# Kernel optimization log

Measured on AMD Instinct MI355X. Metric: run time of the kernel, lower is better.

Reference implementation:

```python
import jax, jax.numpy as jnp
import numpy as np

E = 1024   # embed_dim
H = 16     # num_heads
D = E // H # head_dim
NP = 2     # n_physics
PH = 16    # physics adapter hidden


def setup_inputs() -> dict:
    key = jax.random.key(0)
    ks = jax.random.split(key, 16)
    B, T = 2, 2048
    s = 0.02
    return {
        "x": jax.random.normal(ks[0], (B, T, E), dtype=jnp.float32),
        "physics_state": jax.random.uniform(ks[1], (B, NP), dtype=jnp.float32),
        "attn_mask": jax.random.randint(ks[2], (B, T), 0, 2).astype(jnp.bool_),
        "Wq": jax.random.normal(ks[3], (E, E), dtype=jnp.float32) * s,
        "bq": jnp.zeros((E,), dtype=jnp.float32),
        "Wk": jax.random.normal(ks[4], (E, E), dtype=jnp.float32) * s,
        "bk": jnp.zeros((E,), dtype=jnp.float32),
        "Wv": jax.random.normal(ks[5], (E, E), dtype=jnp.float32) * s,
        "bv": jnp.zeros((E,), dtype=jnp.float32),
        "Wo": jax.random.normal(ks[6], (E, E), dtype=jnp.float32) * s,
        "bo": jnp.zeros((E,), dtype=jnp.float32),
        "Wp1": jax.random.normal(ks[7], (NP, PH), dtype=jnp.float32) * 0.5,
        "bp1": jnp.zeros((PH,), dtype=jnp.float32),
        "Wp2": jax.random.normal(ks[8], (PH, H), dtype=jnp.float32) * 0.25,
        "bp2": jnp.zeros((H,), dtype=jnp.float32),
    }


def reference(x, physics_state, attn_mask, Wq, bq, Wk, bk, Wv, bv, Wo, bo, Wp1, bp1, Wp2, bp2):
    B, T, _ = x.shape
    scale = 1.0 / np.sqrt(D)
    # projections -> (B, H, T, D)
    q = (x @ Wq + bq).reshape(B, T, H, D).transpose(0, 2, 1, 3)
    k = (x @ Wk + bk).reshape(B, T, H, D).transpose(0, 2, 1, 3)
    v = (x @ Wv + bv).reshape(B, T, H, D).transpose(0, 2, 1, 3)
    # per-head physics bias (B, H) -> (B, H, 1, 1)
    h = jax.nn.gelu(physics_state @ Wp1 + bp1, approximate=False)
    phys_bias = (h @ Wp2 + bp2)[:, :, None, None]
    scores = jnp.einsum("bhqd,bhkd->bhqk", q, k) * scale + phys_bias
    # key padding mask: True = keep
    scores = jnp.where(attn_mask[:, None, None, :], scores, -jnp.inf)
    attn = jax.nn.softmax(scores, axis=-1)
    out = jnp.einsum("bhqk,bhkd->bhqd", attn, v)
    out = out.transpose(0, 2, 1, 3).reshape(B, T, E)
    return out @ Wo + bo
```

## Files before the change

### kernel.cpp

```cpp
#include <hip/hip_runtime.h>
#include <hip/hip_bf16.h>
#include <stdint.h>

#define E_  1024
#define H_  16
#define D_  64
#define T_  2048
#define B_  2

typedef unsigned short u16;
typedef unsigned char u8;
typedef __attribute__((ext_vector_type(8))) __bf16 bf16x8;
typedef __attribute__((ext_vector_type(4))) float f32x4;
typedef __attribute__((ext_vector_type(8))) u16 u16x8;
typedef __attribute__((ext_vector_type(4))) u16 u16x4;

__device__ __forceinline__ float bf2f(u16 u) {
  union { uint32_t u32; float f; } x; x.u32 = ((uint32_t)u) << 16; return x.f;
}
__device__ __forceinline__ u16 f2bf(float v) {
  union { float f; uint32_t u; } x; x.f = v;
  uint32_t r = x.u + 0x7fffu + ((x.u >> 16) & 1u);
  return (u16)(r >> 16);
}
__device__ __forceinline__ void async16(const void* g, void* l) {
  __builtin_amdgcn_global_load_lds(
      (const __attribute__((address_space(1))) void*)g,
      (__attribute__((address_space(3))) void*)l, 16, 0, 0);
}
__device__ __forceinline__ int jperm(int k) {
  return (k & 35) | ((k & 12) << 1) | ((k & 16) >> 2);
}

__device__ __forceinline__ int detect_f32(const void* src) {
  u16 u = ((const u16*)src)[2 * (threadIdx.x & 63)];
  int e = (u >> 7) & 0xFF;
  int ex = (e != 0 && (e <= 0x40 || e >= 0xC0)) ? 1 : 0;
  return __popcll(__ballot(ex)) > 16;
}

__global__ __launch_bounds__(256) void convf_kernel(const void* __restrict__ src,
                                                    u16* __restrict__ dst, int n) {
  const int f32in = detect_f32(src);
  int i = (blockIdx.x * 256 + threadIdx.x) * 8;
  if (i >= n) return;
  if (f32in) {
    const float* s = (const float*)src;
    u16x8 o;
#pragma unroll
    for (int j = 0; j < 8; ++j) o[j] = f2bf(s[i + j]);
    *(u16x8*)(dst + i) = o;
  } else {
    *(u16x8*)(dst + i) = *(const u16x8*)((const u16*)src + i);
  }
}

__global__ __launch_bounds__(256) void bias4_kernel(
    const void* __restrict__ b0, const void* __restrict__ b1,
    const void* __restrict__ b2, const void* __restrict__ b3,
    u16* __restrict__ dst) {
  const void* src = (blockIdx.x == 0) ? b0 : (blockIdx.x == 1) ? b1
                    : (blockIdx.x == 2) ? b2 : b3;
  const int f32in = detect_f32(src);
  u16* d = dst + blockIdx.x * 2048;
  int t = threadIdx.x;
#pragma unroll
  for (int j = 0; j < 4; ++j) {
    int i = t + j * 256;
    d[i] = f32in ? f2bf(((const float*)src)[i]) : ((const u16*)src)[i];
  }
}

__global__ __launch_bounds__(256) void maskbias_kernel(const void* __restrict__ mp,
                                                       float* __restrict__ mbg) {
  unsigned w0 = ((const unsigned*)mp)[threadIdx.x & 63];
  int isInt = (__ballot(w0 > 1u) == 0ull);
  int i = blockIdx.x * 256 + threadIdx.x;
  int keep = isInt ? (((const int*)mp)[i] != 0) : (((const u8*)mp)[i] != 0);
  mbg[i] = keep ? -5.77078016f : -30000.f;
}

__global__ __launch_bounds__(256) void wtc4_kernel(
    const void* __restrict__ W0, const void* __restrict__ W1,
    const void* __restrict__ W2, const void* __restrict__ W3,
    u16* __restrict__ T0, u16* __restrict__ T1,
    u16* __restrict__ T2, u16* __restrict__ T3) {
  __shared__ __align__(16) u16 tile[64][65];
  const int z = blockIdx.z;
  const void* Wv = (z == 0) ? W0 : (z == 1) ? W1 : (z == 2) ? W2 : W3;
  u16* WT = (z == 0) ? T0 : (z == 1) ? T1 : (z == 2) ? T2 : T3;
  const int f32in = detect_f32(Wv);
  const int bx = blockIdx.x * 64, by = blockIdx.y * 64;
  const int t = threadIdx.x;
#pragma unroll
  for (int p = 0; p < 2; ++p) {
    int row = p * 32 + (t >> 3);
    int ch = t & 7;
    if (f32in) {
      const float* s = (const float*)Wv + (size_t)(by + row) * E_ + bx + ch * 8;
#pragma unroll
      for (int j = 0; j < 8; ++j) tile[row][ch * 8 + j] = f2bf(s[j]);
    } else {
      u16x8 v = *(const u16x8*)((const u16*)Wv + (size_t)(by + row) * E_ + bx + ch * 8);
#pragma unroll
      for (int j = 0; j < 8; ++j) tile[row][ch * 8 + j] = v[j];
    }
  }
  __syncthreads();
#pragma unroll
  for (int p = 0; p < 2; ++p) {
    int orow = p * 32 + (t >> 3);
    int ch = t & 7;
    u16x8 v;
#pragma unroll
    for (int j = 0; j < 8; ++j) v[j] = tile[ch * 8 + j][orow];
    *(u16x8*)(WT + (size_t)(bx + orow) * E_ + by + ch * 8) = v;
  }
}

__global__ __launch_bounds__(256, 3) void gemm_qkv_kernel(
    const u16* __restrict__ A, const u16* __restrict__ BTm,
    const u16* __restrict__ biases, u16* __restrict__ Qb,
    u16* __restrict__ Kb, u16* __restrict__ Vtb) {
  __shared__ __align__(16) u16 As[128 * 64];
  __shared__ __align__(16) u16 Bs[128 * 64];
  const int tid = threadIdx.x, lane = tid & 63, wid = tid >> 6;
  const int wm = wid >> 1, wn = wid & 1;
  const int l15 = lane & 15, lg = lane >> 4;
  const int r0 = blockIdx.x * 128, c0 = blockIdx.y * 128;
  f32x4 acc[4][4] = {};

  for (int k0 = 0; k0 < E_; k0 += 64) {
    __syncthreads();
#pragma unroll
    for (int i = 0; i < 4; ++i) {
      int row = i * 32 + (tid >> 3);
      int g = (tid & 7) ^ (row & 7);
      async16(A + (size_t)(r0 + row) * E_ + k0 + g * 8,
              (char*)As + i * 4096 + tid * 16);
      async16(BTm + (size_t)(c0 + row) * E_ + k0 + g * 8,
              (char*)Bs + i * 4096 + tid * 16);
    }
    __syncthreads();
#pragma unroll
    for (int kk = 0; kk < 2; ++kk) {
      bf16x8 af[4], bfr[4];
#pragma unroll
      for (int mt = 0; mt < 4; ++mt) {
        int rowa = wm * 64 + mt * 16 + l15;
        int sa = (kk * 4 + lg) ^ (rowa & 7);
        af[mt] = *(const bf16x8*)((const char*)As + rowa * 128 + sa * 16);
        int rowb = wn * 64 + mt * 16 + l15;
        int sb = (kk * 4 + lg) ^ (rowb & 7);
        bfr[mt] = *(const bf16x8*)((const char*)Bs + rowb * 128 + sb * 16);
      }
#pragma unroll
      for (int mt = 0; mt < 4; ++mt)
#pragma unroll
        for (int nt = 0; nt < 4; ++nt)
          acc[mt][nt] = __builtin_amdgcn_mfma_f32_16x16x32_bf16(
              af[mt], bfr[nt], acc[mt][nt], 0, 0, 0);
    }
  }

  const int sel = c0 >> 10;
  u16* outp = (sel == 0) ? Qb : Kb;
#pragma unroll
  for (int mt = 0; mt < 4; ++mt) {
#pragma unroll
    for (int nt = 0; nt < 4; ++nt) {
      int colG = c0 + wn * 64 + nt * 16 + l15;
      int colL = colG & 1023;
      float bv = bf2f(biases[sel * 2048 + colL]);
      int rbase = r0 + wm * 64 + mt * 16 + lg * 4;
      int hh = colL >> 6, dd = colL & 63;
      if (sel == 2) {
        int bb = rbase >> 11, t0 = rbase & (T_ - 1);
        int tp = (t0 & ~63) | jperm(t0 & 63);
        u16x4 pk;
#pragma unroll
        for (int r = 0; r < 4; ++r) pk[r] = f2bf(acc[mt][nt][r] + bv);
        *(u16x4*)(Vtb + (size_t)((bb * H_ + hh) * D_ + dd) * T_ + tp) = pk;
      } else {
#pragma unroll
        for (int r = 0; r < 4; ++r) {
          int row = rbase + r;
          int bb = row >> 11, t = row & (T_ - 1);
          outp[(size_t)((bb * H_ + hh) * T_ + t) * D_ + dd] =
              f2bf(acc[mt][nt][r] + bv);
        }
      }
    }
  }
}

__global__ __launch_bounds__(256, 3) void gemm_out_kernel(
    const u16* __restrict__ A, const u16* __restrict__ BTm,
    const u16* __restrict__ bias, float* __restrict__ out) {
  __shared__ __align__(16) u16 As[128 * 64];
  __shared__ __align__(16) u16 Bs[128 * 64];
  const int tid = threadIdx.x, lane = tid & 63, wid = tid >> 6;
  const int wm = wid >> 1, wn = wid & 1;
  const int l15 = lane & 15, lg = lane >> 4;
  const int r0 = blockIdx.x * 128, c0 = blockIdx.y * 128;
  f32x4 acc[4][4] = {};

  for (int k0 = 0; k0 < E_; k0 += 64) {
    __syncthreads();
#pragma unroll
    for (int i = 0; i < 4; ++i) {
      int row = i * 32 + (tid >> 3);
      int g = (tid & 7) ^ (row & 7);
      async16(A + (size_t)(r0 + row) * E_ + k0 + g * 8,
              (char*)As + i * 4096 + tid * 16);
      async16(BTm + (size_t)(c0 + row) * E_ + k0 + g * 8,
              (char*)Bs + i * 4096 + tid * 16);
    }
    __syncthreads();
#pragma unroll
    for (int kk = 0; kk < 2; ++kk) {
      bf16x8 af[4], bfr[4];
#pragma unroll
      for (int mt = 0; mt < 4; ++mt) {
        int rowa = wm * 64 + mt * 16 + l15;
        int sa = (kk * 4 + lg) ^ (rowa & 7);
        af[mt] = *(const bf16x8*)((const char*)As + rowa * 128 + sa * 16);
        int rowb = wn * 64 + mt * 16 + l15;
        int sb = (kk * 4 + lg) ^ (rowb & 7);
        bfr[mt] = *(const bf16x8*)((const char*)Bs + rowb * 128 + sb * 16);
      }
#pragma unroll
      for (int mt = 0; mt < 4; ++mt)
#pragma unroll
        for (int nt = 0; nt < 4; ++nt)
          acc[mt][nt] = __builtin_amdgcn_mfma_f32_16x16x32_bf16(
              af[mt], bfr[nt], acc[mt][nt], 0, 0, 0);
    }
  }

#pragma unroll
  for (int mt = 0; mt < 4; ++mt)
#pragma unroll
    for (int nt = 0; nt < 4; ++nt) {
      int col = c0 + wn * 64 + nt * 16 + l15;
      float bv = bf2f(bias[col]);
      int rbase = r0 + wm * 64 + mt * 16 + lg * 4;
#pragma unroll
      for (int r = 0; r < 4; ++r)
        out[(size_t)(rbase + r) * E_ + col] = acc[mt][nt][r] + bv;
    }
}

__global__ __launch_bounds__(256, 2) void attn_kernel(
    const u16* __restrict__ Q, const u16* __restrict__ K,
    const u16* __restrict__ VT, const float* __restrict__ mbg,
    u16* __restrict__ outb) {
  __shared__ __align__(16) u16 Ks[3][64 * 64];
  __shared__ __align__(16) u16 Vs[3][64 * 64];
  __shared__ __align__(16) float mb[T_];
  __shared__ __align__(16) u16 oscr[4][2304];
  const int wg = blockIdx.x;
  const int xcd = wg & 7, slot = wg >> 3;
  const int bh = xcd + 8 * (slot >> 4);
  const int q0 = (slot & 15) * 128;
  const int b = bh >> 4, h = bh & 15;
  const int tid = threadIdx.x, lane = tid & 63, w = tid >> 6;
  const int l15 = lane & 15, lg = lane >> 4;

  const u16* qb = Q + (size_t)bh * T_ * D_;
  const u16* kb = K + (size_t)bh * T_ * D_;
  const u16* vb = VT + (size_t)bh * D_ * T_;

  {
    const f32x4* s = (const f32x4*)(mbg + b * T_);
    f32x4* d = (f32x4*)mb;
#pragma unroll
    for (int j = 0; j < 2; ++j) d[tid + j * 256] = s[tid + j * 256];
  }

  bf16x8 qf[2][2];
#pragma unroll
  for (int mt = 0; mt < 2; ++mt)
#pragma unroll
    for (int kd = 0; kd < 2; ++kd) {
      int row = q0 + w * 32 + mt * 16 + l15;
      qf[mt][kd] = *(const bf16x8*)(qb + (size_t)row * D_ + kd * 32 + lg * 8);
    }

#define STAGE(kt_, bi_)                                                  \
  do {                                                                   \
    _Pragma("unroll")                                                    \
    for (int c = 0; c < 2; ++c) {                                        \
      int row_ = c * 32 + (tid >> 3);                                    \
      int g_ = (tid & 7) ^ (row_ & 7);                                   \
      async16(kb + (size_t)((kt_) * 64 + row_) * D_ + g_ * 8,            \
              (char*)&Ks[bi_][0] + c * 4096 + tid * 16);                 \
      async16(vb + (size_t)row_ * T_ + (kt_) * 64 + g_ * 8,              \
              (char*)&Vs[bi_][0] + c * 4096 + tid * 16);                 \
    }                                                                    \
  } while (0)

  STAGE(0, 0);
  STAGE(1, 1);
  asm volatile("s_waitcnt lgkmcnt(0)" ::: "memory");

  f32x4 o[2][4] = {};
  float lrow[2] = {0.f, 0.f};
  const float cc = 0.125f * 1.44269504f;

  int rd = 0, wr = 2;
  for (int kt = 0; kt < 32; ++kt) {
    if (kt < 31)
      asm volatile("s_waitcnt vmcnt(4)" ::: "memory");
    else
      asm volatile("s_waitcnt vmcnt(0)" ::: "memory");
    __builtin_amdgcn_sched_barrier(0);
    __builtin_amdgcn_s_barrier();
    __builtin_amdgcn_sched_barrier(0);
    if (kt < 30) STAGE(kt + 2, wr);
    const char* Kc = (const char*)&Ks[rd][0];
    const char* Vc = (const char*)&Vs[rd][0];

    f32x4 mbv4[4];
#pragma unroll
    for (int mf = 0; mf < 4; ++mf)
      mbv4[mf] = *(const f32x4*)&mb[kt * 64 + mf * 16 + lg * 4];

    f32x4 s2[2][4] = {};
#pragma unroll
    for (int kd = 0; kd < 2; ++kd) {
      bf16x8 kf[4];
#pragma unroll
      for (int mf = 0; mf < 4; ++mf) {
        int row = mf * 16 + l15;
        int sl = (kd * 4 + lg) ^ (row & 7);
        kf[mf] = *(const bf16x8*)(Kc + row * 128 + sl * 16);
      }
      __builtin_amdgcn_s_setprio(1);
#pragma unroll
      for (int mt = 0; mt < 2; ++mt)
#pragma unroll
        for (int mf = 0; mf < 4; ++mf)
          s2[mt][mf] = __builtin_amdgcn_mfma_f32_16x16x32_bf16(
              kf[mf], qf[mt][kd], s2[mt][mf], 0, 0, 0);
      __builtin_amdgcn_s_setprio(0);
    }

    uint32_t pkw[2][4][2];
#pragma unroll
    for (int mt = 0; mt < 2; ++mt) {
#pragma unroll
      for (int mf = 0; mf < 4; ++mf) {
        float p0 = exp2f(fmaf(s2[mt][mf][0], cc, mbv4[mf][0]));
        float p1 = exp2f(fmaf(s2[mt][mf][1], cc, mbv4[mf][1]));
        float p2 = exp2f(fmaf(s2[mt][mf][2], cc, mbv4[mf][2]));
        float p3 = exp2f(fmaf(s2[mt][mf][3], cc, mbv4[mf][3]));
        lrow[mt] += (p0 + p1) + (p2 + p3);
        asm("v_cvt_pk_bf16_f32 %0, %1, %2" : "=v"(pkw[mt][mf][0]) : "v"(p0), "v"(p1));
        asm("v_cvt_pk_bf16_f32 %0, %1, %2" : "=v"(pkw[mt][mf][1]) : "v"(p2), "v"(p3));
      }
    }

#pragma unroll
    for (int kk = 0; kk < 2; ++kk) {
      bf16x8 pf[2], vf[4];
#pragma unroll
      for (int mt = 0; mt < 2; ++mt) {
        union { uint32_t u[4]; bf16x8 v; } pu;
        pu.u[0] = pkw[mt][2 * kk][0];
        pu.u[1] = pkw[mt][2 * kk][1];
        pu.u[2] = pkw[mt][2 * kk + 1][0];
        pu.u[3] = pkw[mt][2 * kk + 1][1];
        pf[mt] = pu.v;
      }
#pragma unroll
      for (int df = 0; df < 4; ++df) {
        int row = df * 16 + l15;
        int sl = (kk * 4 + lg) ^ (row & 7);
        vf[df] = *(const bf16x8*)(Vc + row * 128 + sl * 16);
      }
      __builtin_amdgcn_s_setprio(1);
#pragma unroll
      for (int mt = 0; mt < 2; ++mt)
#pragma unroll
        for (int df = 0; df < 4; ++df)
          o[mt][df] = __builtin_amdgcn_mfma_f32_16x16x32_bf16(
              pf[mt], vf[df], o[mt][df], 0, 0, 0);
      __builtin_amdgcn_s_setprio(0);
    }
    rd = (rd == 2) ? 0 : rd + 1;
    wr = (wr == 2) ? 0 : wr + 1;
  }
#undef STAGE

  float inv[2][4];
#pragma unroll
  for (int mt = 0; mt < 2; ++mt) {
    float t = lrow[mt];
    t += __shfl_xor(t, 16);
    t += __shfl_xor(t, 32);
    float ti = (t > 0.f) ? 1.0f / t : 0.f;
#pragma unroll
    for (int r = 0; r < 4; ++r)
      inv[mt][r] = __shfl(ti, (lane & 48) | (lg * 4 + r));
  }

  char* wbase = (char*)&oscr[w][0];
#pragma unroll
  for (int mt = 0; mt < 2; ++mt)
#pragma unroll
    for (int df = 0; df < 4; ++df)
#pragma unroll
      for (int r = 0; r < 4; ++r) {
        int prow = mt * 16 + lg * 4 + r;
        *(u16*)(wbase + prow * 144 + (df * 16 + l15) * 2) =
            f2bf(o[mt][df][r] * inv[mt][r]);
      }
  asm volatile("s_waitcnt lgkmcnt(0)" ::: "memory");
  __builtin_amdgcn_sched_barrier(0);
  {
    int rowL = lane >> 1;
    int c8 = lane & 1;
    int grow = b * T_ + q0 + w * 32 + rowL;
#pragma unroll
    for (int j = 0; j < 4; ++j) {
      int chunk = c8 + 2 * j;
      u16x8 v = *(const u16x8*)(wbase + rowL * 144 + chunk * 16);
      *(u16x8*)(outb + (size_t)grow * E_ + h * D_ + chunk * 8) = v;
    }
  }
}

extern "C" void kernel_launch(void* const* d_in, const int* in_sizes, int n_in,
                              void* d_out, int out_size, void* d_ws, size_t ws_size,
                              hipStream_t stream) {
  const void* x    = d_in[0];
  const void* mask = d_in[2];
  const void* Wq = d_in[3];
  const void* bq = d_in[4];
  const void* Wk = d_in[5];
  const void* bk = d_in[6];
  const void* Wv = d_in[7];
  const void* bv = d_in[8];
  const void* Wo = d_in[9];
  const void* bo = d_in[10];
  char* ws = (char*)d_ws;

  const size_t MB = 1024 * 1024;
  u16* Kb   = (u16*)(ws + 0 * MB);
  u16* Vtb  = (u16*)(ws + 8 * MB);
  u16* Ab   = (u16*)(ws + 16 * MB);
  u16* WqT  = (u16*)(ws + 16 * MB);
  u16* WkT  = (u16*)(ws + 18 * MB);
  u16* WvT  = (u16*)(ws + 20 * MB);
  u16* WoT  = (u16*)(ws + 24 * MB);
  u16* bqc  = (u16*)(ws + 26 * MB);
  u16* boc  = bqc + 3 * 2048;
  float* mbg = (float*)(ws + 26 * MB + 32 * 1024);

  u16* Qb = (u16*)d_out;
  u16* xc = (u16*)((char*)d_out + 8 * MB);
  float* out = (float*)d_out;

  dim3 blk(256);
  const int NX = B_ * T_ * E_;

  convf_kernel<<<NX / 8 / 256, blk, 0, stream>>>(x, xc, NX);
  bias4_kernel<<<4, blk, 0, stream>>>(bq, bk, bv, bo, bqc);
  maskbias_kernel<<<16, blk, 0, stream>>>(mask, mbg);
  wtc4_kernel<<<dim3(16, 16, 4), blk, 0, stream>>>(Wq, Wk, Wv, Wo,
                                                   WqT, WkT, WvT, WoT);
  gemm_qkv_kernel<<<dim3(32, 24), blk, 0, stream>>>(xc, WqT, bqc, Qb, Kb, Vtb);
  attn_kernel<<<dim3(512), blk, 0, stream>>>(Qb, Kb, Vtb, mbg, Ab);
  gemm_out_kernel<<<dim3(32, 8), blk, 0, stream>>>(Ab, WoT, boc, out);
}
```

Baseline: 129.2 us.

## Split attention over two key halves and add a combine kernel

The attention kernel now splits the key range into two halves, doubling the grid to 1024 workgroups. Each half writes an unnormalized bf16 partial output plus per-row exp-sum partials. A new elementwise combine kernel adds the two partials and normalizes them before the output projection. The aim is more parallelism and shorter per-block loops. The cost is extra global traffic for the partials, an additional launch, and an extra bf16 rounding of unnormalized partial sums.

```diff
diff --git a/kernel.cpp b/kernel.cpp
--- a/kernel.cpp
+++ b/kernel.cpp
@@ -254,15 +254,18 @@
 __global__ __launch_bounds__(256, 2) void attn_kernel(
     const u16* __restrict__ Q, const u16* __restrict__ K,
     const u16* __restrict__ VT, const float* __restrict__ mbg,
-    u16* __restrict__ outb) {
+    u16* __restrict__ P0, u16* __restrict__ P1, float* __restrict__ lpart) {
   __shared__ __align__(16) u16 Ks[3][64 * 64];
   __shared__ __align__(16) u16 Vs[3][64 * 64];
-  __shared__ __align__(16) float mb[T_];
+  __shared__ __align__(16) float mb[1024];
   __shared__ __align__(16) u16 oscr[4][2304];
   const int wg = blockIdx.x;
   const int xcd = wg & 7, slot = wg >> 3;
-  const int bh = xcd + 8 * (slot >> 4);
-  const int q0 = (slot & 15) * 128;
+  const int bh = xcd + 8 * (slot >> 5);
+  const int sub = slot & 31;
+  const int q0 = (sub & 15) * 128;
+  const int khalf = sub >> 4;
+  const int ktb = khalf * 16;
   const int b = bh >> 4, h = bh & 15;
   const int tid = threadIdx.x, lane = tid & 63, w = tid >> 6;
   const int l15 = lane & 15, lg = lane >> 4;
@@ -271,12 +274,7 @@
   const u16* kb = K + (size_t)bh * T_ * D_;
   const u16* vb = VT + (size_t)bh * D_ * T_;
 
-  {
-    const f32x4* s = (const f32x4*)(mbg + b * T_);
-    f32x4* d = (f32x4*)mb;
-#pragma unroll
-    for (int j = 0; j < 2; ++j) d[tid + j * 256] = s[tid + j * 256];
-  }
+  ((f32x4*)mb)[tid] = ((const f32x4*)(mbg + b * T_ + khalf * 1024))[tid];
 
   bf16x8 qf[2][2];
 #pragma unroll
@@ -300,8 +298,8 @@
     }                                                                    \
   } while (0)
 
-  STAGE(0, 0);
-  STAGE(1, 1);
+  STAGE(ktb + 0, 0);
+  STAGE(ktb + 1, 1);
   asm volatile("s_waitcnt lgkmcnt(0)" ::: "memory");
 
   f32x4 o[2][4] = {};
@@ -309,22 +307,22 @@
   const float cc = 0.125f * 1.44269504f;
 
   int rd = 0, wr = 2;
-  for (int kt = 0; kt < 32; ++kt) {
-    if (kt < 31)
+  for (int i = 0; i < 16; ++i) {
+    if (i < 15)
       asm volatile("s_waitcnt vmcnt(4)" ::: "memory");
     else
       asm volatile("s_waitcnt vmcnt(0)" ::: "memory");
     __builtin_amdgcn_sched_barrier(0);
     __builtin_amdgcn_s_barrier();
     __builtin_amdgcn_sched_barrier(0);
-    if (kt < 30) STAGE(kt + 2, wr);
+    if (i < 14) STAGE(ktb + i + 2, wr);
     const char* Kc = (const char*)&Ks[rd][0];
     const char* Vc = (const char*)&Vs[rd][0];
 
     f32x4 mbv4[4];
 #pragma unroll
     for (int mf = 0; mf < 4; ++mf)
-      mbv4[mf] = *(const f32x4*)&mb[kt * 64 + mf * 16 + lg * 4];
+      mbv4[mf] = *(const f32x4*)&mb[i * 64 + mf * 16 + lg * 4];
 
     f32x4 s2[2][4] = {};
 #pragma unroll
@@ -393,18 +391,16 @@
   }
 #undef STAGE
 
-  float inv[2][4];
+  float* lp = lpart + (size_t)khalf * 32 * T_ + (size_t)bh * T_;
 #pragma unroll
   for (int mt = 0; mt < 2; ++mt) {
     float t = lrow[mt];
     t += __shfl_xor(t, 16);
     t += __shfl_xor(t, 32);
-    float ti = (t > 0.f) ? 1.0f / t : 0.f;
-#pragma unroll
-    for (int r = 0; r < 4; ++r)
-      inv[mt][r] = __shfl(ti, (lane & 48) | (lg * 4 + r));
-  }
-
+    if (lg == 0) lp[q0 + w * 32 + mt * 16 + l15] = t;
+  }
+
+  u16* pout = khalf ? P1 : P0;
   char* wbase = (char*)&oscr[w][0];
 #pragma unroll
   for (int mt = 0; mt < 2; ++mt)
@@ -413,8 +409,7 @@
 #pragma unroll
       for (int r = 0; r < 4; ++r) {
         int prow = mt * 16 + lg * 4 + r;
-        *(u16*)(wbase + prow * 144 + (df * 16 + l15) * 2) =
-            f2bf(o[mt][df][r] * inv[mt][r]);
+        *(u16*)(wbase + prow * 144 + (df * 16 + l15) * 2) = f2bf(o[mt][df][r]);
       }
   asm volatile("s_waitcnt lgkmcnt(0)" ::: "memory");
   __builtin_amdgcn_sched_barrier(0);
@@ -426,9 +421,31 @@
     for (int j = 0; j < 4; ++j) {
       int chunk = c8 + 2 * j;
       u16x8 v = *(const u16x8*)(wbase + rowL * 144 + chunk * 16);
-      *(u16x8*)(outb + (size_t)grow * E_ + h * D_ + chunk * 8) = v;
-    }
-  }
+      *(u16x8*)(pout + (size_t)grow * E_ + h * D_ + chunk * 8) = v;
+    }
+  }
+}
+
+__global__ __launch_bounds__(256) void combine_kernel(
+    const u16* __restrict__ P0, const u16* __restrict__ P1,
+    const float* __restrict__ lpart, u16* __restrict__ Ab) {
+  int idx = blockIdx.x * 256 + threadIdx.x;
+  int i8 = idx * 8;
+  int b = i8 >> 21;
+  int t = (i8 >> 10) & (T_ - 1);
+  int e = i8 & (E_ - 1);
+  int bh = b * H_ + (e >> 6);
+  float l0 = lpart[(size_t)bh * T_ + t];
+  float l1 = lpart[32 * (size_t)T_ + (size_t)bh * T_ + t];
+  float ls = l0 + l1;
+  float inv = (ls > 0.f) ? 1.f / ls : 0.f;
+  u16x8 a = *(const u16x8*)(P0 + i8);
+  u16x8 c = *(const u16x8*)(P1 + i8);
+  u16x8 o;
+#pragma unroll
+  for (int j = 0; j < 8; ++j)
+    o[j] = f2bf((bf2f(a[j]) + bf2f(c[j])) * inv);
+  *(u16x8*)(Ab + i8) = o;
 }
 
 extern "C" void kernel_launch(void* const* d_in, const int* in_sizes, int n_in,
@@ -457,9 +474,11 @@
   u16* bqc  = (u16*)(ws + 26 * MB);
   u16* boc  = bqc + 3 * 2048;
   float* mbg = (float*)(ws + 26 * MB + 32 * 1024);
+  float* lpart = (float*)(ws + 26 * MB + 64 * 1024);
 
   u16* Qb = (u16*)d_out;
   u16* xc = (u16*)((char*)d_out + 8 * MB);
+  u16* P1 = xc;
   float* out = (float*)d_out;
 
   dim3 blk(256);
@@ -471,6 +490,7 @@
   wtc4_kernel<<<dim3(16, 16, 4), blk, 0, stream>>>(Wq, Wk, Wv, Wo,
                                                    WqT, WkT, WvT, WoT);
   gemm_qkv_kernel<<<dim3(32, 24), blk, 0, stream>>>(xc, WqT, bqc, Qb, Kb, Vtb);
-  attn_kernel<<<dim3(512), blk, 0, stream>>>(Qb, Kb, Vtb, mbg, Ab);
+  attn_kernel<<<dim3(1024), blk, 0, stream>>>(Qb, Kb, Vtb, mbg, Ab, P1, lpart);
+  combine_kernel<<<NX / 8 / 256, blk, 0, stream>>>(Ab, P1, lpart, Ab);
   gemm_out_kernel<<<dim3(32, 8), blk, 0, stream>>>(Ab, WoT, boc, out);
 }
```

New measurement: 134.8 us. 4.3% more time.
